# Kernel optimization log

Hardware: AMD Instinct MI355X
Metric: run time of the kernel (lower is better)

## Reference

```python
import jax, jax.numpy as jnp
import numpy as np

DIM = 64
HEADS = 8
DIM_HEAD = 64
INNER = HEADS * DIM_HEAD  # 512
MLP = 256
DEPTH = 4
B = 64
HW = 15
NPATCH = HW * HW  # 225
N = NPATCH + 1    # 226 tokens incl cls
SCALE = DIM_HEAD ** -0.5
EPS = 1e-5


def setup_inputs() -> dict:
    key = jax.random.key(0)
    ks = jax.random.split(key, 20)
    s = 0.02
    inp = {
        "hsi": jax.random.normal(ks[0], (B, DIM, HW, HW), jnp.float32),
        "lidar": jax.random.normal(ks[1], (B, DIM, HW, HW), jnp.float32),
        "cls_hsi": jax.random.normal(ks[2], (1, 1, DIM), jnp.float32),
        "cls_lidar": jax.random.normal(ks[3], (1, 1, DIM), jnp.float32),
        "pos_hsi": jax.random.normal(ks[4], (1, N, DIM), jnp.float32),
        "pos_lidar": jax.random.normal(ks[5], (1, N, DIM), jnp.float32),
        "fmg_w": jax.random.normal(ks[6], (2 * DIM, DIM * DIM), jnp.float32) * s,
        "ln1_g": jnp.ones((DEPTH, DIM), jnp.float32),
        "ln1_b": jnp.zeros((DEPTH, DIM), jnp.float32),
        "qkv_w": jax.random.normal(ks[7], (DEPTH, DIM, 3 * INNER), jnp.float32) * s,
        "out_w": jax.random.normal(ks[8], (DEPTH, INNER, DIM), jnp.float32) * s,
        "out_b": jnp.zeros((DEPTH, DIM), jnp.float32),
        "ln2_g": jnp.ones((DEPTH, DIM), jnp.float32),
        "ln2_b": jnp.zeros((DEPTH, DIM), jnp.float32),
        "ff_w1": jax.random.normal(ks[9], (DEPTH, DIM, MLP), jnp.float32) * s,
        "ff_b1": jnp.zeros((DEPTH, MLP), jnp.float32),
        "ff_w2": jax.random.normal(ks[10], (DEPTH, MLP, DIM), jnp.float32) * s,
        "ff_b2": jnp.zeros((DEPTH, DIM), jnp.float32),
    }
    return inp


def _ln(x, g, b):
    m = x.mean(-1, keepdims=True)
    v = ((x - m) ** 2).mean(-1, keepdims=True)
    return (x - m) * jax.lax.rsqrt(v + EPS) * g + b


def _attn(x, dfm, g, b, wqkv, wo, bo):
    # x: [B, N, DIM]; dfm: [B, DIM_HEAD] diagonal of per-sample fusion matrix
    xn = _ln(x, g, b)
    qkv = xn @ wqkv  # [B, N, 3*INNER]
    q, k, v = jnp.split(qkv, 3, axis=-1)
    def heads(t):
        return t.reshape(B, N, HEADS, DIM_HEAD).transpose(0, 2, 1, 3)  # bhnd
    q, v = heads(q), heads(v)
    # torch.einsum('bhnd,bdd->bhnd', q, fm): repeated 'd' in bdd = diagonal of fm
    k = q * dfm[:, None, None, :]
    dots = jnp.einsum('bhid,bhjd->bhij', q, k) * SCALE
    attn = jax.nn.softmax(dots, axis=-1)
    out = jnp.einsum('bhij,bhjd->bhid', attn, v)
    out = out.transpose(0, 2, 1, 3).reshape(B, N, INNER)
    return out @ wo + bo


def _ff(x, g, b, w1, b1, w2, b2):
    xn = _ln(x, g, b)
    h = jax.nn.gelu(xn @ w1 + b1, approximate=False)
    return h @ w2 + b2


def reference(hsi, lidar, cls_hsi, cls_lidar, pos_hsi, pos_lidar, fmg_w,
              ln1_g, ln1_b, qkv_w, out_w, out_b, ln2_g, ln2_b,
              ff_w1, ff_b1, ff_w2, ff_b2):
    # patch_to_embedding with p1=p2=1: b c h w -> b (h w) c
    h_e = hsi.reshape(B, DIM, NPATCH).transpose(0, 2, 1)
    l_e = lidar.reshape(B, DIM, NPATCH).transpose(0, 2, 1)

    # fusion matrix from pre-exchange embeddings
    x = jnp.concatenate([h_e.mean(1), l_e.mean(1)], axis=-1)  # [B, 2*DIM]
    fm = jax.nn.sigmoid(x @ fmg_w).reshape(B, DIM, DIM)
    dfm = jnp.diagonal(fm, axis1=1, axis2=2)  # [B, DIM]

    # _exchange_embedding (faithful to source: reads both halves from hsi)
    n2 = NPATCH // 2
    h_ex = jnp.concatenate([h_e[:, :n2], h_e[:, n2:]], axis=1)
    l_ex = jnp.concatenate([h_e[:, :n2], h_e[:, n2:]], axis=1)

    h_ex = jnp.concatenate([jnp.broadcast_to(cls_hsi, (B, 1, DIM)), h_ex], axis=1)
    l_ex = jnp.concatenate([jnp.broadcast_to(cls_lidar, (B, 1, DIM)), l_ex], axis=1)
    h_ex = h_ex + pos_hsi[:, :N]
    l_ex = l_ex + pos_lidar[:, :N]

    def run_layers(h, l):
        for i in range(DEPTH):
            h = _attn(h, dfm, ln1_g[i], ln1_b[i], qkv_w[i], out_w[i], out_b[i]) + h
            h = _ff(h, ln2_g[i], ln2_b[i], ff_w1[i], ff_b1[i], ff_w2[i], ff_b2[i]) + h
            l = _attn(l, dfm, ln1_g[i], ln1_b[i], qkv_w[i], out_w[i], out_b[i]) + l
            l = _ff(l, ln2_g[i], ln2_b[i], ff_w1[i], ff_b1[i], ff_w2[i], ff_b2[i]) + l
        return h, l

    h_ex, l_ex = run_layers(h_ex, l_ex)

    # _exchange_token: swap cls tokens
    h_new = jnp.concatenate([l_ex[:, :1], h_ex[:, 1:]], axis=1)
    l_new = jnp.concatenate([h_ex[:, :1], l_ex[:, 1:]], axis=1)

    h_new, l_new = run_layers(h_new, l_new)
    return h_new[:, 0] + l_new[:, 0]
```

## Files before the change

### kernel.cpp

```cpp
#include <hip/hip_runtime.h>
#include <hip/hip_bf16.h>
#include <cstdint>

#define NB 64
#define ND 64
#define NH 8
#define DH 64
#define NIN 512
#define NMLP 256
#define NDEPTH 4
#define NPATCH 225
#define NTOK 226
#define NSB 128
#define NROWS (NSB*NTOK)

#define VP 240
#define PBP 40

typedef __attribute__((ext_vector_type(8))) short bfrag8;
typedef __attribute__((ext_vector_type(4))) float ffrag4;

__device__ __forceinline__ unsigned short f2b(float f) {
  uint32_t u; __builtin_memcpy(&u, &f, 4);
  u += 0x7fff + ((u >> 16) & 1);
  return (unsigned short)(u >> 16);
}

__global__ void k_dfm(const float* __restrict__ hsi, const float* __restrict__ lidar,
                      const float* __restrict__ fmg_w, float* __restrict__ sdfm) {
  __shared__ float xc[128];
  int b = blockIdx.x, t = threadIdx.x;
  const float* src = (t < 64) ? hsi : lidar;
  int d = t & 63;
  const float* p = src + ((size_t)b * 64 + d) * NPATCH;
  float s = 0.f;
  for (int i = 0; i < NPATCH; ++i) s += p[i];
  xc[t] = s * (1.0f / 225.0f);
  __syncthreads();
  if (t < 64) {
    float acc = 0.f;
    const float* w = fmg_w + t * 65;
    for (int c = 0; c < 128; ++c) acc += xc[c] * w[c * 4096];
    float sg = 1.0f / (1.0f + expf(-acc));
    sdfm[b * 64 + t] = sqrtf(sg);
  }
}

__global__ void k_build(const float* __restrict__ hsi,
                        const float* __restrict__ cls_h, const float* __restrict__ cls_l,
                        const float* __restrict__ pos_h, const float* __restrict__ pos_l,
                        const float* __restrict__ g, const float* __restrict__ bb,
                        float* __restrict__ X, uint16_t* __restrict__ Xn) {
  int r = blockIdx.x;
  int sb = r / NTOK, n = r - sb * NTOK;
  int s = sb >> 6, b = sb & 63;
  int d = threadIdx.x;
  float v;
  if (n == 0) v = s ? cls_l[d] : cls_h[d];
  else        v = hsi[((size_t)b * 64 + d) * NPATCH + (n - 1)];
  v += (s ? pos_l : pos_h)[n * ND + d];
  X[(size_t)r * ND + d] = v;
  float sm = v, sq = v * v;
  #pragma unroll
  for (int o = 32; o; o >>= 1) { sm += __shfl_xor(sm, o); sq += __shfl_xor(sq, o); }
  float m = sm * (1.f / 64.f);
  float rs = rsqrtf(sq * (1.f / 64.f) - m * m + 1e-5f);
  Xn[(size_t)r * ND + d] = f2b((v - m) * rs * g[d] + bb[d]);
}

__global__ __launch_bounds__(256) void k_wconv(
    const float* __restrict__ qkv_w, const float* __restrict__ out_w,
    const float* __restrict__ ff_w1, const float* __restrict__ ff_w2,
    uint16_t* __restrict__ Wqv, uint16_t* __restrict__ Wo,
    uint16_t* __restrict__ W1, uint16_t* __restrict__ W2) {
  int i = blockIdx.x * 256 + threadIdx.x;
  if (i < 262144) {
    int ly = i >> 16, rem = i & 65535, n = rem >> 6, k = rem & 63;
    int col = n + ((n >> 9) << 9);
    Wqv[i] = f2b(qkv_w[((size_t)ly * 64 + k) * 1536 + col]);
  } else if (i < 393216) {
    int j = i - 262144;
    int ly = j >> 15, rem = j & 32767, n = rem >> 9, k = rem & 511;
    Wo[j] = f2b(out_w[((size_t)ly * 512 + k) * 64 + n]);
  } else if (i < 458752) {
    int j = i - 393216;
    int ly = j >> 14, rem = j & 16383, n = rem >> 6, k = rem & 63;
    W1[j] = f2b(ff_w1[((size_t)ly * 64 + k) * 256 + n]);
  } else {
    int j = i - 458752;
    int ly = j >> 14, rem = j & 16383, n = rem >> 8, k = rem & 255;
    W2[j] = f2b(ff_w2[((size_t)ly * 256 + k) * 64 + n]);
  }
}

__global__ __launch_bounds__(512) void k_fattn(const uint16_t* __restrict__ Xn,
    const uint16_t* __restrict__ Wqv,
    const float* __restrict__ sdfm, uint16_t* __restrict__ Og) {
  __shared__ __align__(16) uint16_t qs[240 * 64];
  __shared__ __align__(16) uint16_t vt[64 * VP];
  __shared__ __align__(16) uint16_t pb[8][16 * PBP];
  int bh = blockIdx.x;
  int sb = bh >> 3, h = bh & 7;
  int t = threadIdx.x, w = t >> 6, l = t & 63;
  int quad = l >> 4, c = l & 15;
  const uint16_t* Xb = Xn + (size_t)sb * NTOK * ND;

  float sf[4];
  #pragma unroll
  for (int dt = 0; dt < 4; ++dt)
    sf[dt] = sdfm[(sb & 63) * 64 + dt * 16 + c] * 0.35355339059327373f;

  for (int it = w; it < 15; it += 8) {
    int i0 = it * 16;
    int ri = i0 + c; if (ri > 225) ri = 225;
    bfrag8 a0 = *(const bfrag8*)(Xb + (size_t)ri * 64 + quad * 8);
    bfrag8 a1 = *(const bfrag8*)(Xb + (size_t)ri * 64 + 32 + quad * 8);
    #pragma unroll
    for (int dt = 0; dt < 4; ++dt) {
      int nq = h * 64 + dt * 16 + c;
      bfrag8 bq0 = *(const bfrag8*)(Wqv + (size_t)nq * 64 + quad * 8);
      bfrag8 bq1 = *(const bfrag8*)(Wqv + (size_t)nq * 64 + 32 + quad * 8);
      ffrag4 zq = {0.f, 0.f, 0.f, 0.f};
      zq = __builtin_amdgcn_mfma_f32_16x16x32_bf16(a0, bq0, zq, 0, 0, 0);
      zq = __builtin_amdgcn_mfma_f32_16x16x32_bf16(a1, bq1, zq, 0, 0, 0);
      bfrag8 bv0 = *(const bfrag8*)(Wqv + (size_t)(512 + nq) * 64 + quad * 8);
      bfrag8 bv1 = *(const bfrag8*)(Wqv + (size_t)(512 + nq) * 64 + 32 + quad * 8);
      ffrag4 zv = {0.f, 0.f, 0.f, 0.f};
      zv = __builtin_amdgcn_mfma_f32_16x16x32_bf16(a0, bv0, zv, 0, 0, 0);
      zv = __builtin_amdgcn_mfma_f32_16x16x32_bf16(a1, bv1, zv, 0, 0, 0);
      int d = dt * 16 + c;
      #pragma unroll
      for (int r = 0; r < 4; ++r) {
        int i = i0 + quad * 4 + r;
        qs[i * 64 + ((((d >> 3) ^ (i & 7))) << 3) + (d & 7)] = f2b(zq[r] * sf[dt]);
        vt[d * VP + i] = f2b(zv[r]);
      }
    }
  }
  __syncthreads();

  uint16_t* pw = &pb[w][0];
  for (int it = w; it < 15; it += 8) {
    int i0 = it * 16;
    int ra = i0 + c, sa = ra & 7;
    bfrag8 a0 = *(const bfrag8*)(qs + ra * 64 + ((quad ^ sa) << 3));
    bfrag8 a1 = *(const bfrag8*)(qs + ra * 64 + (((quad + 4) ^ sa) << 3));
    ffrag4 acc[15];
    #pragma unroll
    for (int jt = 0; jt < 15; ++jt) {
      int rb = jt * 16 + c, sk = rb & 7;
      bfrag8 b0 = *(const bfrag8*)(qs + rb * 64 + ((quad ^ sk) << 3));
      bfrag8 b1 = *(const bfrag8*)(qs + rb * 64 + (((quad + 4) ^ sk) << 3));
      ffrag4 z = {0.f, 0.f, 0.f, 0.f};
      z = __builtin_amdgcn_mfma_f32_16x16x32_bf16(a0, b0, z, 0, 0, 0);
      z = __builtin_amdgcn_mfma_f32_16x16x32_bf16(a1, b1, z, 0, 0, 0);
      acc[jt] = z;
    }
    float rinv[4];
    #pragma unroll
    for (int r = 0; r < 4; ++r) {
      float m = -1e30f;
      #pragma unroll
      for (int jt = 0; jt < 15; ++jt) m = fmaxf(m, acc[jt][r]);
      #pragma unroll
      for (int o = 8; o; o >>= 1) m = fmaxf(m, __shfl_xor(m, o));
      float s = 0.f;
      #pragma unroll
      for (int jt = 0; jt < 15; ++jt) {
        float p = __expf(acc[jt][r] - m);
        if (jt == 14 && c >= 2) p = 0.f;
        acc[jt][r] = p;
        s += p;
      }
      #pragma unroll
      for (int o = 8; o; o >>= 1) s += __shfl_xor(s, o);
      rinv[r] = 1.f / s;
    }
    ffrag4 oa[4];
    #pragma unroll
    for (int dt = 0; dt < 4; ++dt) oa[dt] = (ffrag4){0.f, 0.f, 0.f, 0.f};
    for (int jc = 0; jc < 8; ++jc) {
      if (jc == 7) {
        *(unsigned long long*)(pw + c * PBP + 16 + quad * 4) = 0ull;
      }
      #pragma unroll
      for (int r = 0; r < 4; ++r) {
        int row = quad * 4 + r;
        pw[row * PBP + c] = f2b(acc[2 * jc][r]);
        if (jc < 7) pw[row * PBP + 16 + c] = f2b(acc[2 * jc + 1][r]);
      }
      bfrag8 pa = *(const bfrag8*)(pw + c * PBP + quad * 8);
      int j0 = jc * 32;
      #pragma unroll
      for (int dt = 0; dt < 4; ++dt) {
        bfrag8 vb;
        if (jc < 7)
          vb = *(const bfrag8*)(vt + (dt * 16 + c) * VP + j0 + quad * 8);
        else
          vb = *(const bfrag8*)(vt + (dt * 16 + c) * VP + 224 + (quad & 1) * 8);
        oa[dt] = __builtin_amdgcn_mfma_f32_16x16x32_bf16(pa, vb, oa[dt], 0, 0, 0);
      }
    }
    #pragma unroll
    for (int dt = 0; dt < 4; ++dt) {
      #pragma unroll
      for (int r = 0; r < 4; ++r) {
        int i = i0 + quad * 4 + r;
        if (i < NTOK)
          Og[((size_t)sb * NTOK + i) * NIN + h * DH + dt * 16 + c] =
              f2b(oa[dt][r] * rinv[r]);
      }
    }
  }
}

__global__ __launch_bounds__(64) void k_pf(const uint16_t* __restrict__ Og,
    const uint16_t* __restrict__ Wot,
    const float* __restrict__ bo, float* __restrict__ X,
    const float* __restrict__ g2, const float* __restrict__ bb2,
    const uint16_t* __restrict__ W1t,
    const float* __restrict__ b1,
    const uint16_t* __restrict__ W2t,
    const float* __restrict__ b2,
    const float* __restrict__ gn, const float* __restrict__ bbn,
    uint16_t* __restrict__ XnOut) {
  __shared__ __align__(16) uint16_t xa2[16 * 72];
  __shared__ __align__(16) uint16_t ha[16 * 264];
  int t = threadIdx.x;
  int quad = t >> 4, c = t & 15;
  int r0 = blockIdx.x * 16;

  const uint16_t* orow = Og + (size_t)(r0 + c) * 512 + quad * 8;
  bfrag8 a[16];
  #pragma unroll
  for (int kc = 0; kc < 16; ++kc) a[kc] = *(const bfrag8*)(orow + kc * 32);
  ffrag4 acc[4];
  #pragma unroll
  for (int jt = 0; jt < 4; ++jt) acc[jt] = (ffrag4){0.f, 0.f, 0.f, 0.f};
  #pragma unroll
  for (int kc = 0; kc < 16; ++kc) {
    #pragma unroll
    for (int jt = 0; jt < 4; ++jt) {
      bfrag8 b = *(const bfrag8*)(Wot + (size_t)(jt * 16 + c) * 512 + kc * 32 + quad * 8);
      acc[jt] = __builtin_amdgcn_mfma_f32_16x16x32_bf16(a[kc], b, acc[jt], 0, 0, 0);
    }
  }
  float xv[4][4];
  #pragma unroll
  for (int jt = 0; jt < 4; ++jt) {
    float bv = bo[jt * 16 + c];
    #pragma unroll
    for (int r = 0; r < 4; ++r) {
      int il = quad * 4 + r;
      size_t idx = (size_t)(r0 + il) * 64 + jt * 16 + c;
      float v = X[idx] + acc[jt][r] + bv;
      X[idx] = v;
      xv[jt][r] = v;
    }
  }
  #pragma unroll
  for (int r = 0; r < 4; ++r) {
    float s = xv[0][r] + xv[1][r] + xv[2][r] + xv[3][r];
    float q = xv[0][r]*xv[0][r] + xv[1][r]*xv[1][r] + xv[2][r]*xv[2][r] + xv[3][r]*xv[3][r];
    #pragma unroll
    for (int o = 8; o; o >>= 1) { s += __shfl_xor(s, o); q += __shfl_xor(q, o); }
    float m = s * (1.f / 64.f);
    float rs = rsqrtf(q * (1.f / 64.f) - m * m + 1e-5f);
    int il = quad * 4 + r;
    #pragma unroll
    for (int jt = 0; jt < 4; ++jt) {
      int n = jt * 16 + c;
      xa2[il * 72 + n] = f2b((xv[jt][r] - m) * rs * g2[n] + bb2[n]);
    }
  }
  const uint16_t* xrow = xa2 + c * 72;
  bfrag8 a0 = *(const bfrag8*)(xrow + quad * 8);
  bfrag8 a1 = *(const bfrag8*)(xrow + 32 + quad * 8);
  ffrag4 acc1[16];
  #pragma unroll
  for (int jt = 0; jt < 16; ++jt) {
    bfrag8 b0  = *(const bfrag8*)(W1t + (size_t)(jt * 16 + c) * 64 + quad * 8);
    bfrag8 b1f = *(const bfrag8*)(W1t + (size_t)(jt * 16 + c) * 64 + 32 + quad * 8);
    ffrag4 z = {0.f, 0.f, 0.f, 0.f};
    z = __builtin_amdgcn_mfma_f32_16x16x32_bf16(a0, b0, z, 0, 0, 0);
    z = __builtin_amdgcn_mfma_f32_16x16x32_bf16(a1, b1f, z, 0, 0, 0);
    acc1[jt] = z;
  }
  #pragma unroll
  for (int jt = 0; jt < 16; ++jt) {
    float bv = b1[jt * 16 + c];
    #pragma unroll
    for (int r = 0; r < 4; ++r) {
      float z = acc1[jt][r] + bv;
      float hg = 0.5f * z * (1.f + erff(z * 0.7071067811865476f));
      ha[(quad * 4 + r) * 264 + jt * 16 + c] = f2b(hg);
    }
  }
  ffrag4 o2[4];
  #pragma unroll
  for (int jt = 0; jt < 4; ++jt) o2[jt] = (ffrag4){0.f, 0.f, 0.f, 0.f};
  #pragma unroll
  for (int kc = 0; kc < 8; ++kc) {
    bfrag8 pa = *(const bfrag8*)(ha + c * 264 + kc * 32 + quad * 8);
    #pragma unroll
    for (int jt = 0; jt < 4; ++jt) {
      bfrag8 vb = *(const bfrag8*)(W2t + (size_t)(jt * 16 + c) * 256 + kc * 32 + quad * 8);
      o2[jt] = __builtin_amdgcn_mfma_f32_16x16x32_bf16(pa, vb, o2[jt], 0, 0, 0);
    }
  }
  float yv[4][4];
  #pragma unroll
  for (int jt = 0; jt < 4; ++jt) {
    float bv = b2[jt * 16 + c];
    #pragma unroll
    for (int r = 0; r < 4; ++r) {
      int il = quad * 4 + r;
      size_t idx = (size_t)(r0 + il) * 64 + jt * 16 + c;
      float v = X[idx] + o2[jt][r] + bv;
      X[idx] = v;
      yv[jt][r] = v;
    }
  }
  #pragma unroll
  for (int r = 0; r < 4; ++r) {
    float s = yv[0][r] + yv[1][r] + yv[2][r] + yv[3][r];
    float q = yv[0][r]*yv[0][r] + yv[1][r]*yv[1][r] + yv[2][r]*yv[2][r] + yv[3][r]*yv[3][r];
    #pragma unroll
    for (int o = 8; o; o >>= 1) { s += __shfl_xor(s, o); q += __shfl_xor(q, o); }
    float m = s * (1.f / 64.f);
    float rs = rsqrtf(q * (1.f / 64.f) - m * m + 1e-5f);
    int il = quad * 4 + r;
    #pragma unroll
    for (int jt = 0; jt < 4; ++jt) {
      int n = jt * 16 + c;
      XnOut[(size_t)(r0 + il) * 64 + n] = f2b((yv[jt][r] - m) * rs * gn[n] + bbn[n]);
    }
  }
}

__global__ void k_xchg(float* __restrict__ X, uint16_t* __restrict__ Xn,
                       const float* __restrict__ g, const float* __restrict__ bb) {
  int b = blockIdx.x, d = threadIdx.x;
  size_t i0 = (size_t)(b * NTOK) * ND + d;
  size_t i1 = (size_t)((64 + b) * NTOK) * ND + d;
  float a = X[i0], cc = X[i1];
  X[i0] = cc; X[i1] = a;
  float s0 = cc, q0 = cc * cc, s1 = a, q1 = a * a;
  #pragma unroll
  for (int o = 32; o; o >>= 1) {
    s0 += __shfl_xor(s0, o); q0 += __shfl_xor(q0, o);
    s1 += __shfl_xor(s1, o); q1 += __shfl_xor(q1, o);
  }
  float m0 = s0 * (1.f / 64.f), rs0 = rsqrtf(q0 * (1.f / 64.f) - m0 * m0 + 1e-5f);
  float m1 = s1 * (1.f / 64.f), rs1 = rsqrtf(q1 * (1.f / 64.f) - m1 * m1 + 1e-5f);
  Xn[i0] = f2b((cc - m0) * rs0 * g[d] + bb[d]);
  Xn[i1] = f2b((a - m1) * rs1 * g[d] + bb[d]);
}

__global__ void k_out(const float* __restrict__ X, float* __restrict__ out) {
  int i = blockIdx.x * 64 + threadIdx.x;
  int b = i >> 6, d = i & 63;
  out[i] = X[(size_t)b * NTOK * ND + d] + X[(size_t)(64 + b) * NTOK * ND + d];
}

extern "C" void kernel_launch(void* const* d_in, const int* in_sizes, int n_in,
                              void* d_out, int out_size, void* d_ws, size_t ws_size,
                              hipStream_t stream) {
  const float* hsi   = (const float*)d_in[0];
  const float* lidar = (const float*)d_in[1];
  const float* cls_h = (const float*)d_in[2];
  const float* cls_l = (const float*)d_in[3];
  const float* pos_h = (const float*)d_in[4];
  const float* pos_l = (const float*)d_in[5];
  const float* fmg_w = (const float*)d_in[6];
  const float* ln1_g = (const float*)d_in[7];
  const float* ln1_b = (const float*)d_in[8];
  const float* qkv_w = (const float*)d_in[9];
  const float* out_w = (const float*)d_in[10];
  const float* out_b = (const float*)d_in[11];
  const float* ln2_g = (const float*)d_in[12];
  const float* ln2_b = (const float*)d_in[13];
  const float* ff_w1 = (const float*)d_in[14];
  const float* ff_b1 = (const float*)d_in[15];
  const float* ff_w2 = (const float*)d_in[16];
  const float* ff_b2 = (const float*)d_in[17];

  char* ws = (char*)d_ws;
  float*    X    = (float*)ws;
  float*    sdfm = (float*)(ws + 7405568);
  uint16_t* Xn   = (uint16_t*)(ws + 7421952);
  uint16_t* Og   = (uint16_t*)(ws + 11124736);
  uint16_t* Wqv  = (uint16_t*)(ws + 40747008);
  uint16_t* Wo   = (uint16_t*)(ws + 41271296);
  uint16_t* W1   = (uint16_t*)(ws + 41533440);
  uint16_t* W2   = (uint16_t*)(ws + 41664512);

  k_wconv<<<2048, 256, 0, stream>>>(qkv_w, out_w, ff_w1, ff_w2, Wqv, Wo, W1, W2);
  k_dfm<<<NB, 128, 0, stream>>>(hsi, lidar, fmg_w, sdfm);
  k_build<<<NROWS, 64, 0, stream>>>(hsi, cls_h, cls_l, pos_h, pos_l,
                                    ln1_g, ln1_b, X, Xn);
  for (int pass = 0; pass < 2; ++pass) {
    for (int ly = 0; ly < NDEPTH; ++ly) {
      int nx = (ly + 1) & 3;
      k_fattn<<<NSB * NH, 512, 0, stream>>>(Xn, Wqv + (size_t)ly * 65536, sdfm, Og);
      k_pf<<<NROWS / 16, 64, 0, stream>>>(Og, Wo + (size_t)ly * 32768, out_b + ly * ND,
                                          X, ln2_g + ly * ND, ln2_b + ly * ND,
                                          W1 + (size_t)ly * 16384, ff_b1 + ly * NMLP,
                                          W2 + (size_t)ly * 16384, ff_b2 + ly * ND,
                                          ln1_g + nx * ND, ln1_b + nx * ND, Xn);
    }
    if (pass == 0) k_xchg<<<64, 64, 0, stream>>>(X, Xn, ln1_g, ln1_b);
  }
  k_out<<<64, 64, 0, stream>>>(X, (float*)d_out);
}
```

Before: 805.7 us.

## Split post-attention FFN kernel across two waves per 16-row block

After: 805.4 us. No clear change (-0.0%).

```diff
diff --git a/kernel.cpp b/kernel.cpp
--- a/kernel.cpp
+++ b/kernel.cpp
@@ -16,6 +16,7 @@
 
 #define VP 240
 #define PBP 40
+
 
 typedef __attribute__((ext_vector_type(8))) short bfrag8;
 typedef __attribute__((ext_vector_type(4))) float ffrag4;
@@ -214,7 +215,7 @@
   }
 }
 
-__global__ __launch_bounds__(64) void k_pf(const uint16_t* __restrict__ Og,
+__global__ __launch_bounds__(128) void k_pf(const uint16_t* __restrict__ Og,
     const uint16_t* __restrict__ Wot,
     const float* __restrict__ bo, float* __restrict__ X,
     const float* __restrict__ g2, const float* __restrict__ bb2,
@@ -226,114 +227,136 @@
     uint16_t* __restrict__ XnOut) {
   __shared__ __align__(16) uint16_t xa2[16 * 72];
   __shared__ __align__(16) uint16_t ha[16 * 264];
+  __shared__ float lnp[2][16][2];
   int t = threadIdx.x;
-  int quad = t >> 4, c = t & 15;
+  int w = t >> 6, l = t & 63;
+  int quad = l >> 4, c = l & 15;
   int r0 = blockIdx.x * 16;
 
   const uint16_t* orow = Og + (size_t)(r0 + c) * 512 + quad * 8;
   bfrag8 a[16];
   #pragma unroll
   for (int kc = 0; kc < 16; ++kc) a[kc] = *(const bfrag8*)(orow + kc * 32);
-  ffrag4 acc[4];
-  #pragma unroll
-  for (int jt = 0; jt < 4; ++jt) acc[jt] = (ffrag4){0.f, 0.f, 0.f, 0.f};
+  ffrag4 acc[2][2];
+  #pragma unroll
+  for (int j = 0; j < 2; ++j)
+    #pragma unroll
+    for (int p = 0; p < 2; ++p) acc[j][p] = (ffrag4){0.f, 0.f, 0.f, 0.f};
   #pragma unroll
   for (int kc = 0; kc < 16; ++kc) {
     #pragma unroll
-    for (int jt = 0; jt < 4; ++jt) {
+    for (int j = 0; j < 2; ++j) {
+      int jt = 2 * w + j;
       bfrag8 b = *(const bfrag8*)(Wot + (size_t)(jt * 16 + c) * 512 + kc * 32 + quad * 8);
-      acc[jt] = __builtin_amdgcn_mfma_f32_16x16x32_bf16(a[kc], b, acc[jt], 0, 0, 0);
-    }
-  }
-  float xv[4][4];
-  #pragma unroll
-  for (int jt = 0; jt < 4; ++jt) {
+      acc[j][kc & 1] = __builtin_amdgcn_mfma_f32_16x16x32_bf16(a[kc], b, acc[j][kc & 1], 0, 0, 0);
+    }
+  }
+  float xv[2][4];
+  #pragma unroll
+  for (int j = 0; j < 2; ++j) {
+    int jt = 2 * w + j;
     float bv = bo[jt * 16 + c];
     #pragma unroll
     for (int r = 0; r < 4; ++r) {
       int il = quad * 4 + r;
       size_t idx = (size_t)(r0 + il) * 64 + jt * 16 + c;
-      float v = X[idx] + acc[jt][r] + bv;
+      float v = X[idx] + (acc[j][0][r] + acc[j][1][r]) + bv;
       X[idx] = v;
-      xv[jt][r] = v;
+      xv[j][r] = v;
     }
   }
   #pragma unroll
   for (int r = 0; r < 4; ++r) {
-    float s = xv[0][r] + xv[1][r] + xv[2][r] + xv[3][r];
-    float q = xv[0][r]*xv[0][r] + xv[1][r]*xv[1][r] + xv[2][r]*xv[2][r] + xv[3][r]*xv[3][r];
+    float s = xv[0][r] + xv[1][r];
+    float q = xv[0][r] * xv[0][r] + xv[1][r] * xv[1][r];
     #pragma unroll
     for (int o = 8; o; o >>= 1) { s += __shfl_xor(s, o); q += __shfl_xor(q, o); }
+    if (c == 0) { lnp[w][quad * 4 + r][0] = s; lnp[w][quad * 4 + r][1] = q; }
+  }
+  __syncthreads();
+  #pragma unroll
+  for (int r = 0; r < 4; ++r) {
+    int il = quad * 4 + r;
+    float s = lnp[0][il][0] + lnp[1][il][0];
+    float q = lnp[0][il][1] + lnp[1][il][1];
     float m = s * (1.f / 64.f);
     float rs = rsqrtf(q * (1.f / 64.f) - m * m + 1e-5f);
-    int il = quad * 4 + r;
-    #pragma unroll
-    for (int jt = 0; jt < 4; ++jt) {
-      int n = jt * 16 + c;
-      xa2[il * 72 + n] = f2b((xv[jt][r] - m) * rs * g2[n] + bb2[n]);
-    }
-  }
+    #pragma unroll
+    for (int j = 0; j < 2; ++j) {
+      int n = (2 * w + j) * 16 + c;
+      xa2[il * 72 + n] = f2b((xv[j][r] - m) * rs * g2[n] + bb2[n]);
+    }
+  }
+  __syncthreads();
   const uint16_t* xrow = xa2 + c * 72;
   bfrag8 a0 = *(const bfrag8*)(xrow + quad * 8);
   bfrag8 a1 = *(const bfrag8*)(xrow + 32 + quad * 8);
-  ffrag4 acc1[16];
-  #pragma unroll
-  for (int jt = 0; jt < 16; ++jt) {
+  #pragma unroll
+  for (int jj = 0; jj < 8; ++jj) {
+    int jt = 8 * w + jj;
     bfrag8 b0  = *(const bfrag8*)(W1t + (size_t)(jt * 16 + c) * 64 + quad * 8);
     bfrag8 b1f = *(const bfrag8*)(W1t + (size_t)(jt * 16 + c) * 64 + 32 + quad * 8);
     ffrag4 z = {0.f, 0.f, 0.f, 0.f};
     z = __builtin_amdgcn_mfma_f32_16x16x32_bf16(a0, b0, z, 0, 0, 0);
     z = __builtin_amdgcn_mfma_f32_16x16x32_bf16(a1, b1f, z, 0, 0, 0);
-    acc1[jt] = z;
-  }
-  #pragma unroll
-  for (int jt = 0; jt < 16; ++jt) {
     float bv = b1[jt * 16 + c];
     #pragma unroll
     for (int r = 0; r < 4; ++r) {
-      float z = acc1[jt][r] + bv;
-      float hg = 0.5f * z * (1.f + erff(z * 0.7071067811865476f));
+      float zz = z[r] + bv;
+      float hg = 0.5f * zz * (1.f + erff(zz * 0.7071067811865476f));
       ha[(quad * 4 + r) * 264 + jt * 16 + c] = f2b(hg);
     }
   }
-  ffrag4 o2[4];
-  #pragma unroll
-  for (int jt = 0; jt < 4; ++jt) o2[jt] = (ffrag4){0.f, 0.f, 0.f, 0.f};
+  __syncthreads();
+  ffrag4 o2[2][2];
+  #pragma unroll
+  for (int j = 0; j < 2; ++j)
+    #pragma unroll
+    for (int p = 0; p < 2; ++p) o2[j][p] = (ffrag4){0.f, 0.f, 0.f, 0.f};
   #pragma unroll
   for (int kc = 0; kc < 8; ++kc) {
     bfrag8 pa = *(const bfrag8*)(ha + c * 264 + kc * 32 + quad * 8);
     #pragma unroll
-    for (int jt = 0; jt < 4; ++jt) {
+    for (int j = 0; j < 2; ++j) {
+      int jt = 2 * w + j;
       bfrag8 vb = *(const bfrag8*)(W2t + (size_t)(jt * 16 + c) * 256 + kc * 32 + quad * 8);
-      o2[jt] = __builtin_amdgcn_mfma_f32_16x16x32_bf16(pa, vb, o2[jt], 0, 0, 0);
-    }
-  }
-  float yv[4][4];
-  #pragma unroll
-  for (int jt = 0; jt < 4; ++jt) {
+      o2[j][kc & 1] = __builtin_amdgcn_mfma_f32_16x16x32_bf16(pa, vb, o2[j][kc & 1], 0, 0, 0);
+    }
+  }
+  float yv[2][4];
+  #pragma unroll
+  for (int j = 0; j < 2; ++j) {
+    int jt = 2 * w + j;
     float bv = b2[jt * 16 + c];
     #pragma unroll
     for (int r = 0; r < 4; ++r) {
       int il = quad * 4 + r;
       size_t idx = (size_t)(r0 + il) * 64 + jt * 16 + c;
-      float v = X[idx] + o2[jt][r] + bv;
+      float v = X[idx] + (o2[j][0][r] + o2[j][1][r]) + bv;
       X[idx] = v;
-      yv[jt][r] = v;
+      yv[j][r] = v;
     }
   }
   #pragma unroll
   for (int r = 0; r < 4; ++r) {
-    float s = yv[0][r] + yv[1][r] + yv[2][r] + yv[3][r];
-    float q = yv[0][r]*yv[0][r] + yv[1][r]*yv[1][r] + yv[2][r]*yv[2][r] + yv[3][r]*yv[3][r];
+    float s = yv[0][r] + yv[1][r];
+    float q = yv[0][r] * yv[0][r] + yv[1][r] * yv[1][r];
     #pragma unroll
     for (int o = 8; o; o >>= 1) { s += __shfl_xor(s, o); q += __shfl_xor(q, o); }
+    if (c == 0) { lnp[w][quad * 4 + r][0] = s; lnp[w][quad * 4 + r][1] = q; }
+  }
+  __syncthreads();
+  #pragma unroll
+  for (int r = 0; r < 4; ++r) {
+    int il = quad * 4 + r;
+    float s = lnp[0][il][0] + lnp[1][il][0];
+    float q = lnp[0][il][1] + lnp[1][il][1];
     float m = s * (1.f / 64.f);
     float rs = rsqrtf(q * (1.f / 64.f) - m * m + 1e-5f);
-    int il = quad * 4 + r;
-    #pragma unroll
-    for (int jt = 0; jt < 4; ++jt) {
-      int n = jt * 16 + c;
-      XnOut[(size_t)(r0 + il) * 64 + n] = f2b((yv[jt][r] - m) * rs * gn[n] + bbn[n]);
+    #pragma unroll
+    for (int j = 0; j < 2; ++j) {
+      int n = (2 * w + j) * 16 + c;
+      XnOut[(size_t)(r0 + il) * 64 + n] = f2b((yv[j][r] - m) * rs * gn[n] + bbn[n]);
     }
   }
 }
@@ -403,11 +426,11 @@
     for (int ly = 0; ly < NDEPTH; ++ly) {
       int nx = (ly + 1) & 3;
       k_fattn<<<NSB * NH, 512, 0, stream>>>(Xn, Wqv + (size_t)ly * 65536, sdfm, Og);
-      k_pf<<<NROWS / 16, 64, 0, stream>>>(Og, Wo + (size_t)ly * 32768, out_b + ly * ND,
-                                          X, ln2_g + ly * ND, ln2_b + ly * ND,
-                                          W1 + (size_t)ly * 16384, ff_b1 + ly * NMLP,
-                                          W2 + (size_t)ly * 16384, ff_b2 + ly * ND,
-                                          ln1_g + nx * ND, ln1_b + nx * ND, Xn);
+      k_pf<<<NROWS / 16, 128, 0, stream>>>(Og, Wo + (size_t)ly * 32768, out_b + ly * ND,
+                                           X, ln2_g + ly * ND, ln2_b + ly * ND,
+                                           W1 + (size_t)ly * 16384, ff_b1 + ly * NMLP,
+                                           W2 + (size_t)ly * 16384, ff_b2 + ly * ND,
+                                           ln1_g + nx * ND, ln1_b + nx * ND, Xn);
     }
     if (pass == 0) k_xchg<<<64, 64, 0, stream>>>(X, Xn, ln1_g, ln1_b);
   }
```
